# Kernel tuning notes

Hardware: AMD Instinct MI355X
Metric: run time of the kernel (lower is better)

Reference implementation:

```python
import jax, jax.numpy as jnp
import numpy as np

T = 10          # time_steps
IN_DIM = 784    # 28*28
HID = 256
NCLS = 47
THRESH = 1.0
TAU_MEM = 2.0   # LIF membrane time constant
TAU_OUT = 2.0   # readout EMA time constant


@jax.custom_vjp
def spike_fn(u):
    # Heaviside spike on (v - threshold), surrogate gradient in bwd.
    return (u >= 0.0).astype(u.dtype)

def _spike_fwd(u):
    return spike_fn(u), u

def _spike_bwd(u, g):
    # sigmoid surrogate derivative, slope 4
    s = jax.nn.sigmoid(4.0 * u)
    return (g * 4.0 * s * (1.0 - s),)

spike_fn.defvjp(_spike_fwd, _spike_bwd)


def setup_inputs() -> dict:
    key = jax.random.key(0)
    k1, k2, k3 = jax.random.split(key, 3)
    x = jax.random.uniform(k1, (4096, 1, 28, 28), dtype=jnp.float32)
    W1 = jax.random.normal(k2, (IN_DIM, HID), dtype=jnp.float32) / np.float32(np.sqrt(IN_DIM))
    b1 = jnp.zeros((HID,), jnp.float32)
    Wr = jax.random.normal(k3, (HID, NCLS), dtype=jnp.float32) / np.float32(np.sqrt(HID))
    br = jnp.zeros((NCLS,), jnp.float32)
    return {"x": x, "W1": W1, "b1": b1, "Wr": Wr, "br": br}


def reference(x, W1, b1, Wr, br):
    B = x.shape[0]
    xf = x.reshape(B, -1)  # [B, 784] pixel intensities in [0,1]
    # rate_encode_flat: Bernoulli(p=pixel) spikes per timestep -> [T, B, 784]
    ek = jax.random.key(42)
    seq = (jax.random.uniform(ek, (T, B, IN_DIM), dtype=xf.dtype) < xf[None]).astype(xf.dtype)

    def step(carry, s_t):
        v_hid, v_out = carry
        I_hid = s_t @ W1 + b1                      # [B, HID]
        v_hid = v_hid + (I_hid - v_hid) / TAU_MEM  # leaky integration
        spk = spike_fn(v_hid - THRESH)             # spike emission
        v_hid = v_hid * (1.0 - spk)                # hard reset to 0
        I = spk @ Wr + br                          # [B, NCLS]
        v_out = v_out + (I - v_out) / TAU_OUT      # output EMA
        return (v_hid, v_out), None

    init = (jnp.zeros((B, HID), xf.dtype), jnp.zeros((B, NCLS), xf.dtype))
    (_, v_out), _ = jax.lax.scan(step, init, seq)
    return v_out
```

## Files before the change

### kernel.cpp

```cpp
#include <hip/hip_runtime.h>
#include <stdint.h>


#define T_STEPS 10
#define BATCH   4096
#define IN_DIM  784
#define HID     256
#define NCLS    47
#define NROWS   (T_STEPS * BATCH)
#define KWORDS  25
#define KPAD    800

#define WS_IALL_OFF 0u
#define WS_W1HI_OFF 46039040u
#define WS_W1MD_OFF (46039040u + 409600u)
#define WS_W1LO_OFF (46039040u + 819200u)

typedef __attribute__((ext_vector_type(8))) short    bf16x8;
typedef __attribute__((ext_vector_type(4))) float    f32x4;
typedef __attribute__((ext_vector_type(4))) uint32_t u32x4;

__device__ __forceinline__ uint32_t rotl32(uint32_t x, uint32_t r) {
    return __builtin_amdgcn_alignbit(x, x, 32u - r);
}

__device__ __forceinline__ uint32_t tf_hash(uint32_t lo) {
    const uint32_t ks1 = 42u;
    const uint32_t ks2 = 0x1BD11BDAu ^ 42u;
    uint32_t x0 = 0u;
    uint32_t x1 = lo + ks1;
#define TF_RND(r) { x0 += x1; x1 = rotl32(x1, r); x1 ^= x0; }
    TF_RND(13) TF_RND(15) TF_RND(26) TF_RND(6)
    x0 += ks1; x1 += ks2 + 1u;
    TF_RND(17) TF_RND(29) TF_RND(16) TF_RND(24)
    x0 += ks2; x1 += 2u;
    TF_RND(13) TF_RND(15) TF_RND(26) TF_RND(6)
    x1 += ks1 + 3u;
    TF_RND(17) TF_RND(29) TF_RND(16) TF_RND(24)
    x0 += ks1; x1 += ks2 + 4u;
    TF_RND(13) TF_RND(15) TF_RND(26) TF_RND(6)
    x0 += ks2; x1 += 5u;
#undef TF_RND
    return x0 ^ x1;
}

__global__ __launch_bounds__(256) void splitk_k(
        const float* __restrict__ W1, ushort* __restrict__ hiT,
        ushort* __restrict__ midT, ushort* __restrict__ loT) {
    int n = blockIdx.x;
    for (int k = threadIdx.x; k < KPAD; k += 256) {
        float w = (k < IN_DIM) ? W1[k * HID + n] : 0.0f;
        uint32_t u = __float_as_uint(w);
        uint32_t hb = (u + 0x7FFFu + ((u >> 16) & 1u)) >> 16;
        float hf = __uint_as_float(hb << 16);
        float r1 = w - hf;
        uint32_t u1 = __float_as_uint(r1);
        uint32_t mb = (u1 + 0x7FFFu + ((u1 >> 16) & 1u)) >> 16;
        float mf2 = __uint_as_float(mb << 16);
        float r2 = r1 - mf2;
        uint32_t u2 = __float_as_uint(r2);
        uint32_t lb = (u2 + 0x7FFFu + ((u2 >> 16) & 1u)) >> 16;
        hiT [n * KPAD + k] = (ushort)hb;
        midT[n * KPAD + k] = (ushort)mb;
        loT [n * KPAD + k] = (ushort)lb;
    }
}

#define LDS_A  0
#define LDS_BH 4096
#define LDS_BM 20480
#define LDS_BL 36864

__global__ __launch_bounds__(256, 3) void fused_gemm_k(
        const ushort* __restrict__ hiT, const ushort* __restrict__ midT,
        const ushort* __restrict__ loT, const float* __restrict__ b1,
        const float* __restrict__ x, float* __restrict__ I_all) {
    __shared__ __align__(16) char lds[53248];

    const int tid = threadIdx.x;
    const int l   = tid & 63;
    const int wv  = tid >> 6;
    const int t   = blockIdx.x >> 6;
    const int b0  = (blockIdx.x & 63) << 6;
    const int m0  = blockIdx.x << 6;

    f32x4 acc[4][4] = {};

    const int q   = l >> 4;
    const int sig = q ^ (l & 3) ^ ((l >> 2) & 3);
    const int a_base = LDS_A + ((l & 15) << 6) + (sig << 4);
    const int b_off  = (((wv << 6) + (l & 15)) << 6) + (sig << 4);

    const ushort* hi_p[4];
    const ushort* md_p[4];
    const ushort* lo_p[4];
    int ldst_c[4];
#pragma unroll
    for (int i = 0; i < 4; ++i) {
        int s  = (wv << 8) + (i << 6) + l;
        int n  = s >> 2;
        int qs = s & 3;
        int qd = qs ^ (n & 3) ^ ((n >> 2) & 3);
        size_t eoff = (size_t)n * KPAD + ((size_t)qd << 3);
        hi_p[i] = hiT  + eoff;
        md_p[i] = midT + eoff;
        lo_p[i] = loT  + eoff;
        ldst_c[i] = ((wv << 8) + (i << 6)) << 4;
    }

    const int er = tid >> 2;
    const int eq = tid & 3;
    const int ea = LDS_A + (er << 6) + ((eq ^ (er & 3) ^ ((er >> 2) & 3)) << 4);
    const int row_b = b0 + er;
    const float* xp = x + (size_t)row_b * IN_DIM + (eq << 3);
    uint32_t ib = (uint32_t)(row_b * IN_DIM) + (uint32_t)(eq << 3)
                + (uint32_t)t * (uint32_t)(BATCH * IN_DIM);

    for (int kw = 0; kw < KWORDS; ++kw) {
        __syncthreads();

#pragma unroll
        for (int i = 0; i < 4; ++i) {
            __builtin_amdgcn_global_load_lds(
                (const __attribute__((address_space(1))) void*)hi_p[i],
                (__attribute__((address_space(3))) void*)(lds + LDS_BH + ldst_c[i]),
                16, 0, 0);
            __builtin_amdgcn_global_load_lds(
                (const __attribute__((address_space(1))) void*)md_p[i],
                (__attribute__((address_space(3))) void*)(lds + LDS_BM + ldst_c[i]),
                16, 0, 0);
            __builtin_amdgcn_global_load_lds(
                (const __attribute__((address_space(1))) void*)lo_p[i],
                (__attribute__((address_space(3))) void*)(lds + LDS_BL + ldst_c[i]),
                16, 0, 0);
            hi_p[i] += 32;  md_p[i] += 32;  lo_p[i] += 32;
        }

        {
            u32x4 v = {0u, 0u, 0u, 0u};
            if (!(kw == 24 && eq >= 2)) {
                float4 xa = *(const float4*)xp;
                float4 xb = *(const float4*)(xp + 4);
                uint32_t c0 = ((float)(tf_hash(ib + 0u) >> 9) < xa.x * 8388608.0f) ? 0x3F80u : 0u;
                uint32_t c1 = ((float)(tf_hash(ib + 1u) >> 9) < xa.y * 8388608.0f) ? 0x3F800000u : 0u;
                uint32_t c2 = ((float)(tf_hash(ib + 2u) >> 9) < xa.z * 8388608.0f) ? 0x3F80u : 0u;
                uint32_t c3 = ((float)(tf_hash(ib + 3u) >> 9) < xa.w * 8388608.0f) ? 0x3F800000u : 0u;
                uint32_t c4 = ((float)(tf_hash(ib + 4u) >> 9) < xb.x * 8388608.0f) ? 0x3F80u : 0u;
                uint32_t c5 = ((float)(tf_hash(ib + 5u) >> 9) < xb.y * 8388608.0f) ? 0x3F800000u : 0u;
                uint32_t c6 = ((float)(tf_hash(ib + 6u) >> 9) < xb.z * 8388608.0f) ? 0x3F80u : 0u;
                uint32_t c7 = ((float)(tf_hash(ib + 7u) >> 9) < xb.w * 8388608.0f) ? 0x3F800000u : 0u;
                v.x = c0 | c1;  v.y = c2 | c3;  v.z = c4 | c5;  v.w = c6 | c7;
            }
            *(u32x4*)(lds + ea) = v;
        }
        xp += 32;  ib += 32u;

        __syncthreads();

        bf16x8 af[4];
#pragma unroll
        for (int mt = 0; mt < 4; ++mt)
            af[mt] = *(const bf16x8*)(lds + a_base + (mt << 10));
#pragma unroll
        for (int nt = 0; nt < 4; ++nt) {
            bf16x8 bh = *(const bf16x8*)(lds + LDS_BH + b_off + (nt << 10));
            bf16x8 bm = *(const bf16x8*)(lds + LDS_BM + b_off + (nt << 10));
            bf16x8 bl = *(const bf16x8*)(lds + LDS_BL + b_off + (nt << 10));
#pragma unroll
            for (int mt = 0; mt < 4; ++mt) {
                acc[mt][nt] = __builtin_amdgcn_mfma_f32_16x16x32_bf16(af[mt], bh, acc[mt][nt], 0, 0, 0);
                acc[mt][nt] = __builtin_amdgcn_mfma_f32_16x16x32_bf16(af[mt], bm, acc[mt][nt], 0, 0, 0);
                acc[mt][nt] = __builtin_amdgcn_mfma_f32_16x16x32_bf16(af[mt], bl, acc[mt][nt], 0, 0, 0);
            }
        }
    }

    const int c0 = l & 15;
    float b1v[4];
#pragma unroll
    for (int nt = 0; nt < 4; ++nt)
        b1v[nt] = b1[(wv << 6) + (nt << 4) + c0];
#pragma unroll
    for (int mt = 0; mt < 4; ++mt) {
#pragma unroll
        for (int nt = 0; nt < 4; ++nt) {
            int col = (wv << 6) + (nt << 4) + c0;
#pragma unroll
            for (int r = 0; r < 4; ++r) {
                int row = m0 + (mt << 4) + (q << 2) + r;
                I_all[(size_t)row * HID + col] = acc[mt][nt][r] + b1v[nt];
            }
        }
    }
}

__global__ __launch_bounds__(256) void scanout_k(
        const float* __restrict__ I_all, const float* __restrict__ Wr,
        const float* __restrict__ br, float* __restrict__ out) {
    __shared__ float gl[16 * 256];
    const int tid = threadIdx.x;
    const int b0  = blockIdx.x << 4;

#pragma unroll 4
    for (int b = 0; b < 16; ++b) {
        const float* p = I_all + ((size_t)(b0 + b) << 8) + tid;
        float v = 0.f, ga = 0.f, wt = 0.0009765625f;
#pragma unroll
        for (int t = 0; t < T_STEPS; ++t) {
            float I = p[(size_t)t * BATCH * HID];
            v = v + (I - v) * 0.5f;
            if (v >= 1.0f) { ga += wt; v = 0.f; }
            wt += wt;
        }
        gl[(b << 8) + tid] = ga;
    }
    __syncthreads();

    const int wv = tid >> 6;
    const int c  = tid & 63;
    if (c >= NCLS) return;
    float acc[4] = {0.f, 0.f, 0.f, 0.f};
    for (int h4 = 0; h4 < 64; ++h4) {
        float w0 = Wr[((h4 << 2) + 0) * NCLS + c];
        float w1 = Wr[((h4 << 2) + 1) * NCLS + c];
        float w2 = Wr[((h4 << 2) + 2) * NCLS + c];
        float w3 = Wr[((h4 << 2) + 3) * NCLS + c];
#pragma unroll
        for (int j = 0; j < 4; ++j) {
            float4 gg = *(float4*)&gl[(((wv << 2) + j) << 8) + (h4 << 2)];
            acc[j] = fmaf(gg.x, w0, acc[j]);
            acc[j] = fmaf(gg.y, w1, acc[j]);
            acc[j] = fmaf(gg.z, w2, acc[j]);
            acc[j] = fmaf(gg.w, w3, acc[j]);
        }
    }
    float brv = br[c] * 0.9990234375f;
#pragma unroll
    for (int j = 0; j < 4; ++j)
        out[(b0 + (wv << 2) + j) * NCLS + c] = acc[j] + brv;
}

extern "C" void kernel_launch(void* const* d_in, const int* in_sizes, int n_in,
                              void* d_out, int out_size, void* d_ws, size_t ws_size,
                              hipStream_t stream) {
    const float* x  = (const float*)d_in[0];
    const float* W1 = (const float*)d_in[1];
    const float* b1 = (const float*)d_in[2];
    const float* Wr = (const float*)d_in[3];
    const float* br = (const float*)d_in[4];
    float* out = (float*)d_out;

    float*  I_all = (float*) ((char*)d_ws + WS_IALL_OFF);
    ushort* w1hi  = (ushort*)((char*)d_ws + WS_W1HI_OFF);
    ushort* w1md  = (ushort*)((char*)d_ws + WS_W1MD_OFF);
    ushort* w1lo  = (ushort*)((char*)d_ws + WS_W1LO_OFF);

    splitk_k<<<HID, 256, 0, stream>>>(W1, w1hi, w1md, w1lo);
    fused_gemm_k<<<NROWS / 64, 256, 0, stream>>>(w1hi, w1md, w1lo, b1, x, I_all);
    scanout_k<<<BATCH / 16, 256, 0, stream>>>(I_all, Wr, br, out);
}
```

Measured before the change: 199.6 us.

## Precompute Bernoulli spikes as packed bitmasks in a separate kernel; shrink scanout blocks

Moves the threefry hash and Bernoulli comparison out of the MFMA GEMM loop into a dedicated spikegen kernel. That kernel writes one 32-bit bitmask per row per 32-column K-chunk, and the GEMM prefetches and expands these words into bf16 ones/zeros in LDS. The goal is to take the ALU-heavy RNG off the GEMM critical path and spread it across a fully parallel grid. The cost is an extra launch and about 4 MB of workspace traffic. Separately, scanout now handles 4 batch rows per block instead of 16, giving four times as many blocks.

```diff
diff --git a/kernel.cpp b/kernel.cpp
--- a/kernel.cpp
+++ b/kernel.cpp
@@ -12,6 +12,7 @@
 #define KPAD    800
 
 #define WS_IALL_OFF 0u
+#define WS_SPK_OFF  41943040u
 #define WS_W1HI_OFF 46039040u
 #define WS_W1MD_OFF (46039040u + 409600u)
 #define WS_W1LO_OFF (46039040u + 819200u)
@@ -66,6 +67,34 @@
     }
 }
 
+__global__ __launch_bounds__(256) void spikegen_k(
+        const float* __restrict__ x, uint32_t* __restrict__ spk) {
+    const int kw  = blockIdx.y;
+    const int row = (blockIdx.x << 8) + threadIdx.x;
+    const int b   = row & (BATCH - 1);
+    const int k0  = kw << 5;
+    const float* xp = x + (size_t)b * IN_DIM + k0;
+    const uint32_t ib = (uint32_t)row * (uint32_t)IN_DIM + (uint32_t)k0;
+    const int ng = (kw == KWORDS - 1) ? 2 : 4;
+    uint32_t wbits = 0u;
+    for (int g = 0; g < ng; ++g) {
+        float4 xa = *(const float4*)(xp + (g << 3));
+        float4 xb = *(const float4*)(xp + (g << 3) + 4);
+        uint32_t base = ib + (uint32_t)(g << 3);
+        uint32_t bits = 0u;
+        bits |= ((float)(tf_hash(base + 0u) >> 9) < xa.x * 8388608.0f) ? 1u   : 0u;
+        bits |= ((float)(tf_hash(base + 1u) >> 9) < xa.y * 8388608.0f) ? 2u   : 0u;
+        bits |= ((float)(tf_hash(base + 2u) >> 9) < xa.z * 8388608.0f) ? 4u   : 0u;
+        bits |= ((float)(tf_hash(base + 3u) >> 9) < xa.w * 8388608.0f) ? 8u   : 0u;
+        bits |= ((float)(tf_hash(base + 4u) >> 9) < xb.x * 8388608.0f) ? 16u  : 0u;
+        bits |= ((float)(tf_hash(base + 5u) >> 9) < xb.y * 8388608.0f) ? 32u  : 0u;
+        bits |= ((float)(tf_hash(base + 6u) >> 9) < xb.z * 8388608.0f) ? 64u  : 0u;
+        bits |= ((float)(tf_hash(base + 7u) >> 9) < xb.w * 8388608.0f) ? 128u : 0u;
+        wbits |= bits << (g << 3);
+    }
+    spk[(size_t)kw * NROWS + row] = wbits;
+}
+
 #define LDS_A  0
 #define LDS_BH 4096
 #define LDS_BM 20480
@@ -74,14 +103,12 @@
 __global__ __launch_bounds__(256, 3) void fused_gemm_k(
         const ushort* __restrict__ hiT, const ushort* __restrict__ midT,
         const ushort* __restrict__ loT, const float* __restrict__ b1,
-        const float* __restrict__ x, float* __restrict__ I_all) {
+        const uint32_t* __restrict__ spk, float* __restrict__ I_all) {
     __shared__ __align__(16) char lds[53248];
 
     const int tid = threadIdx.x;
     const int l   = tid & 63;
     const int wv  = tid >> 6;
-    const int t   = blockIdx.x >> 6;
-    const int b0  = (blockIdx.x & 63) << 6;
     const int m0  = blockIdx.x << 6;
 
     f32x4 acc[4][4] = {};
@@ -111,10 +138,9 @@
     const int er = tid >> 2;
     const int eq = tid & 3;
     const int ea = LDS_A + (er << 6) + ((eq ^ (er & 3) ^ ((er >> 2) & 3)) << 4);
-    const int row_b = b0 + er;
-    const float* xp = x + (size_t)row_b * IN_DIM + (eq << 3);
-    uint32_t ib = (uint32_t)(row_b * IN_DIM) + (uint32_t)(eq << 3)
-                + (uint32_t)t * (uint32_t)(BATCH * IN_DIM);
+
+    const uint32_t* sp = spk + (size_t)(m0 + er);
+    uint32_t wcur = sp[0];
 
     for (int kw = 0; kw < KWORDS; ++kw) {
         __syncthreads();
@@ -136,24 +162,18 @@
             hi_p[i] += 32;  md_p[i] += 32;  lo_p[i] += 32;
         }
 
+        sp += NROWS;
+        uint32_t wnext = (kw < KWORDS - 1) ? sp[0] : 0u;
+
         {
-            u32x4 v = {0u, 0u, 0u, 0u};
-            if (!(kw == 24 && eq >= 2)) {
-                float4 xa = *(const float4*)xp;
-                float4 xb = *(const float4*)(xp + 4);
-                uint32_t c0 = ((float)(tf_hash(ib + 0u) >> 9) < xa.x * 8388608.0f) ? 0x3F80u : 0u;
-                uint32_t c1 = ((float)(tf_hash(ib + 1u) >> 9) < xa.y * 8388608.0f) ? 0x3F800000u : 0u;
-                uint32_t c2 = ((float)(tf_hash(ib + 2u) >> 9) < xa.z * 8388608.0f) ? 0x3F80u : 0u;
-                uint32_t c3 = ((float)(tf_hash(ib + 3u) >> 9) < xa.w * 8388608.0f) ? 0x3F800000u : 0u;
-                uint32_t c4 = ((float)(tf_hash(ib + 4u) >> 9) < xb.x * 8388608.0f) ? 0x3F80u : 0u;
-                uint32_t c5 = ((float)(tf_hash(ib + 5u) >> 9) < xb.y * 8388608.0f) ? 0x3F800000u : 0u;
-                uint32_t c6 = ((float)(tf_hash(ib + 6u) >> 9) < xb.z * 8388608.0f) ? 0x3F80u : 0u;
-                uint32_t c7 = ((float)(tf_hash(ib + 7u) >> 9) < xb.w * 8388608.0f) ? 0x3F800000u : 0u;
-                v.x = c0 | c1;  v.y = c2 | c3;  v.z = c4 | c5;  v.w = c6 | c7;
-            }
+            uint32_t byt = (wcur >> (eq << 3)) & 0xffu;
+            u32x4 v;
+            v.x = ((byt & 1u)   ? 0x3F80u : 0u) | ((byt & 2u)   ? 0x3F800000u : 0u);
+            v.y = ((byt & 4u)   ? 0x3F80u : 0u) | ((byt & 8u)   ? 0x3F800000u : 0u);
+            v.z = ((byt & 16u)  ? 0x3F80u : 0u) | ((byt & 32u)  ? 0x3F800000u : 0u);
+            v.w = ((byt & 64u)  ? 0x3F80u : 0u) | ((byt & 128u) ? 0x3F800000u : 0u);
             *(u32x4*)(lds + ea) = v;
         }
-        xp += 32;  ib += 32u;
 
         __syncthreads();
 
@@ -173,6 +193,7 @@
                 acc[mt][nt] = __builtin_amdgcn_mfma_f32_16x16x32_bf16(af[mt], bl, acc[mt][nt], 0, 0, 0);
             }
         }
+        wcur = wnext;
     }
 
     const int c0 = l & 15;
@@ -197,12 +218,12 @@
 __global__ __launch_bounds__(256) void scanout_k(
         const float* __restrict__ I_all, const float* __restrict__ Wr,
         const float* __restrict__ br, float* __restrict__ out) {
-    __shared__ float gl[16 * 256];
+    __shared__ float gl[4 * 256];
     const int tid = threadIdx.x;
-    const int b0  = blockIdx.x << 4;
-
-#pragma unroll 4
-    for (int b = 0; b < 16; ++b) {
+    const int b0  = blockIdx.x << 2;
+
+#pragma unroll
+    for (int b = 0; b < 4; ++b) {
         const float* p = I_all + ((size_t)(b0 + b) << 8) + tid;
         float v = 0.f, ga = 0.f, wt = 0.0009765625f;
 #pragma unroll
@@ -219,25 +240,21 @@
     const int wv = tid >> 6;
     const int c  = tid & 63;
     if (c >= NCLS) return;
-    float acc[4] = {0.f, 0.f, 0.f, 0.f};
+    const float* gb = &gl[wv << 8];
+    float acc = 0.f;
     for (int h4 = 0; h4 < 64; ++h4) {
         float w0 = Wr[((h4 << 2) + 0) * NCLS + c];
         float w1 = Wr[((h4 << 2) + 1) * NCLS + c];
         float w2 = Wr[((h4 << 2) + 2) * NCLS + c];
         float w3 = Wr[((h4 << 2) + 3) * NCLS + c];
-#pragma unroll
-        for (int j = 0; j < 4; ++j) {
-            float4 gg = *(float4*)&gl[(((wv << 2) + j) << 8) + (h4 << 2)];
-            acc[j] = fmaf(gg.x, w0, acc[j]);
-            acc[j] = fmaf(gg.y, w1, acc[j]);
-            acc[j] = fmaf(gg.z, w2, acc[j]);
-            acc[j] = fmaf(gg.w, w3, acc[j]);
-        }
+        float4 gg = *(const float4*)&gb[h4 << 2];
+        acc = fmaf(gg.x, w0, acc);
+        acc = fmaf(gg.y, w1, acc);
+        acc = fmaf(gg.z, w2, acc);
+        acc = fmaf(gg.w, w3, acc);
     }
     float brv = br[c] * 0.9990234375f;
-#pragma unroll
-    for (int j = 0; j < 4; ++j)
-        out[(b0 + (wv << 2) + j) * NCLS + c] = acc[j] + brv;
+    out[(b0 + wv) * NCLS + c] = acc + brv;
 }
 
 extern "C" void kernel_launch(void* const* d_in, const int* in_sizes, int n_in,
@@ -250,12 +267,14 @@
     const float* br = (const float*)d_in[4];
     float* out = (float*)d_out;
 
-    float*  I_all = (float*) ((char*)d_ws + WS_IALL_OFF);
-    ushort* w1hi  = (ushort*)((char*)d_ws + WS_W1HI_OFF);
-    ushort* w1md  = (ushort*)((char*)d_ws + WS_W1MD_OFF);
-    ushort* w1lo  = (ushort*)((char*)d_ws + WS_W1LO_OFF);
+    float*    I_all = (float*)   ((char*)d_ws + WS_IALL_OFF);
+    uint32_t* spkw  = (uint32_t*)((char*)d_ws + WS_SPK_OFF);
+    ushort*   w1hi  = (ushort*)  ((char*)d_ws + WS_W1HI_OFF);
+    ushort*   w1md  = (ushort*)  ((char*)d_ws + WS_W1MD_OFF);
+    ushort*   w1lo  = (ushort*)  ((char*)d_ws + WS_W1LO_OFF);
 
     splitk_k<<<HID, 256, 0, stream>>>(W1, w1hi, w1md, w1lo);
-    fused_gemm_k<<<NROWS / 64, 256, 0, stream>>>(w1hi, w1md, w1lo, b1, x, I_all);
-    scanout_k<<<BATCH / 16, 256, 0, stream>>>(I_all, Wr, br, out);
-}
+    spikegen_k<<<dim3(NROWS / 256, KWORDS), 256, 0, stream>>>(x, spkw);
+    fused_gemm_k<<<NROWS / 64, 256, 0, stream>>>(w1hi, w1md, w1lo, b1, spkw, I_all);
+    scanout_k<<<BATCH / 4, 256, 0, stream>>>(I_all, Wr, br, out);
+}
```

Result: slower. 216.6 us (+8.5%).
